# Kernel tuning notes

Measured on AMD Instinct MI355X. Metric: run time of the kernel, lower is better.

## Reference

```python
import jax, jax.numpy as jnp
import numpy as np

N_NODES = 20000   # len(set(idx_i)); edge targets cover all nodes
N_EDGES = 320000
F = 128           # feature dim f
N_RBF = 20        # n radial basis functions
R_CUT = 5.0


def setup_inputs() -> dict:
    key = jax.random.key(0)
    ks = jax.random.split(key, 8)
    s = jax.random.normal(ks[0], (N_EDGES, 1, F), dtype=jnp.float32)
    r = jax.random.normal(ks[1], (N_EDGES, 3), dtype=jnp.float32)
    v = jax.random.normal(ks[2], (N_EDGES, 3, F), dtype=jnp.float32)
    idx_i = jax.random.randint(ks[3], (N_EDGES,), 0, N_NODES, dtype=jnp.int32)
    W_phi = jax.random.normal(ks[4], (F, 3 * F), dtype=jnp.float32) * 0.05
    b_phi = jnp.zeros((3 * F,), dtype=jnp.float32)
    W_w = jax.random.normal(ks[5], (N_RBF, 3 * F), dtype=jnp.float32) * 0.05
    b_w = jnp.zeros((3 * F,), dtype=jnp.float32)
    return {"s": s, "r": r, "v": v, "idx_i": idx_i,
            "W_phi": W_phi, "b_phi": b_phi, "W_w": W_w, "b_w": b_w}


def reference(s, r, v, idx_i, W_phi, b_phi, W_w, b_w):
    # phi network: [E,1,F] -> [E,1,3F]
    phi_out = jnp.einsum('eif,fg->eig', s, W_phi) + b_phi

    # RBF on edge vector norms: [E,1,1] -> [E,1,n]
    r_norm = jnp.linalg.norm(r, axis=1, keepdims=True)[:, :, None]  # [E,1,1]
    n_vals = jnp.arange(1, N_RBF + 1, dtype=jnp.float32)            # [n]
    rbf = jnp.sin(n_vals * (jnp.pi / R_CUT) * r_norm) / r_norm      # [E,1,n]
    # cosine cutoff applied to rbf values (faithful to source)
    rbf = jnp.where(rbf <= R_CUT,
                    0.5 * (jnp.cos(jnp.pi * rbf / R_CUT) + 1.0),
                    jnp.zeros_like(rbf))

    # w network: [E,1,n] -> [E,1,3F]
    w = jnp.einsum('ein,ng->eig', rbf, W_w) + b_w

    split = w * phi_out                    # [E,1,3F]
    sp0 = split[..., :F]                   # gates v
    sp1 = split[..., F:2 * F]              # scalar message
    sp2 = split[..., 2 * F:]               # gates direction

    # scatter-add scalar messages -> [N,1,F]
    out_s = jax.ops.segment_sum(sp1, idx_i, num_segments=N_NODES)

    # direction term: detached r, normalized by GLOBAL Frobenius norm (faithful)
    org_r = jax.lax.stop_gradient(r)
    org_r = org_r / jnp.linalg.norm(org_r)         # [E,3]
    dir_msg = sp2 * org_r[:, :, None]              # [E,3,F]
    v_msg = dir_msg + sp0 * v                      # [E,3,F]

    # scatter-add vector messages -> [N,3,F]
    out_v = jax.ops.segment_sum(v_msg, idx_i, num_segments=N_NODES)
    return out_v, out_s
```

## Files before the change

### kernel.cpp

```cpp
#include <hip/hip_runtime.h>
#include <hip/hip_bf16.h>
#include <math.h>

#define E_TOT   320000
#define NNODE   20000
#define FDIM    128
#define N3F     384
#define NRBF    20
#define OV_SIZE (NNODE * 3 * FDIM)

typedef __attribute__((ext_vector_type(8))) short short8;
typedef __attribute__((ext_vector_type(4))) short short4v;
typedef __attribute__((ext_vector_type(4))) float f32x4;

__device__ __forceinline__ short f2bf(float x) {
  union { float f; unsigned u; } v; v.f = x;
  unsigned r = (v.u + 0x7fffu + ((v.u >> 16) & 1u)) >> 16;
  return (short)r;
}

__global__ void sumsq_kernel(const float* __restrict__ r, float* __restrict__ ws, int n) {
  int tid = blockIdx.x * blockDim.x + threadIdx.x;
  float acc = 0.f;
  for (int i = tid; i < n; i += gridDim.x * blockDim.x) {
    float x = r[i];
    acc += x * x;
  }
  for (int off = 32; off > 0; off >>= 1) acc += __shfl_down(acc, off);
  __shared__ float s[4];
  int lane = threadIdx.x & 63, w = threadIdx.x >> 6;
  if (lane == 0) s[w] = acc;
  __syncthreads();
  if (threadIdx.x == 0) {
    float t = s[0] + s[1] + s[2] + s[3];
    unsafeAtomicAdd(ws, t);
  }
}

__global__ void prep_kernel(const float* __restrict__ Wphi, const float* __restrict__ Ww,
                            short* __restrict__ frag) {
  int g = blockIdx.x * 256 + threadIdx.x;
  int lane = g & 63;
  int fid  = g >> 6;
  short* out = frag + (size_t)g * 8;
  if (fid < 96) {
    int ntile = fid >> 2, ks = fid & 3;
    int n  = ntile * 16 + (lane & 15);
    int kb = ks * 32 + (lane >> 4) * 8;
#pragma unroll
    for (int j = 0; j < 8; ++j) out[j] = f2bf(Wphi[(kb + j) * N3F + n]);
  } else if (fid < 120) {
    int ntile = fid - 96;
    int n  = ntile * 16 + (lane & 15);
    int kb = (lane >> 4) * 8;
#pragma unroll
    for (int j = 0; j < 8; ++j) {
      int k = kb + j;
      out[j] = (k < NRBF) ? f2bf(Ww[k * N3F + n]) : (short)0;
    }
  }
}

__launch_bounds__(256, 2)
__global__ void main_kernel(const float* __restrict__ s_in, const float* __restrict__ r_in,
                            const float* __restrict__ v_in, const int* __restrict__ idx_in,
                            const float* __restrict__ bphi_in, const float* __restrict__ bw_in,
                            const short* __restrict__ frag, const float* __restrict__ ws_sumsq,
                            float* __restrict__ out) {
  __shared__ __align__(16) short sh_s[64 * 136];
  __shared__ __align__(16) short sh_rbf[64 * 40];
  __shared__ float sh_bphi[N3F];
  __shared__ float sh_bw[N3F];
  __shared__ float sh_orgr[64][4];
  __shared__ int   sh_idx[64];

  const int tid = threadIdx.x;
  const int e0  = blockIdx.x * 64;
  const float inv_gnorm = 1.0f / sqrtf(ws_sumsq[0]);

  const float4* s4 = (const float4*)(s_in + (size_t)e0 * FDIM);
#pragma unroll
  for (int it = 0; it < 8; ++it) {
    int idx4 = tid + it * 256;
    float4 val = s4[idx4];
    int e = idx4 >> 5, kq = idx4 & 31;
    short4v p = { f2bf(val.x), f2bf(val.y), f2bf(val.z), f2bf(val.w) };
    *(short4v*)&sh_s[e * 136 + kq * 4] = p;
  }
  for (int j = tid; j < N3F; j += 256) {
    sh_bphi[j] = bphi_in[j];
    sh_bw[j]   = bw_in[j];
  }
  if (tid < 64) {
    int e = e0 + tid;
    sh_idx[tid] = idx_in[e];
    float rx = r_in[e * 3 + 0], ry = r_in[e * 3 + 1], rz = r_in[e * 3 + 2];
    float rn = sqrtf(rx * rx + ry * ry + rz * rz);
    float irn = 1.0f / rn;
    sh_orgr[tid][0] = rx * inv_gnorm;
    sh_orgr[tid][1] = ry * inv_gnorm;
    sh_orgr[tid][2] = rz * inv_gnorm;
    const float c0 = 0.62831853071795864769f;
#pragma unroll
    for (int n = 1; n <= NRBF; ++n) {
      float t = sinf(((float)n * c0) * rn) * irn;
      float val = (t <= 5.0f) ? 0.5f * (cosf(c0 * t) + 1.0f) : 0.0f;
      sh_rbf[tid * 40 + (n - 1)] = f2bf(val);
    }
#pragma unroll
    for (int k = NRBF; k < 32; ++k) sh_rbf[tid * 40 + k] = 0;
  }
  __syncthreads();

  const int wave = tid >> 6, lane = tid & 63;
  const int col  = lane & 15;
  const int q    = lane >> 4;

  const int arow = wave * 16 + col;
  short8 a_phi[4];
#pragma unroll
  for (int ks = 0; ks < 4; ++ks)
    a_phi[ks] = *(const short8*)&sh_s[arow * 136 + ks * 32 + q * 8];
  short8 a_w = *(const short8*)&sh_rbf[arow * 40 + q * 8];

  int   nidx[4]; int erow[4];
  float orx[4], ory[4], orz[4];
#pragma unroll
  for (int i = 0; i < 4; ++i) {
    int el = wave * 16 + q * 4 + i;
    erow[i] = el;
    nidx[i] = sh_idx[el];
    orx[i] = sh_orgr[el][0];
    ory[i] = sh_orgr[el][1];
    orz[i] = sh_orgr[el][2];
  }

  float* out_v = out;
  float* out_s = out + OV_SIZE;
  const short8* fp = (const short8*)frag;
  const short8* fw = fp + 96 * 64;

  for (int f = 0; f < 8; ++f) {
    const int nt0 = f, nt1 = f + 8, nt2 = f + 16;
    f32x4 accP0 = {0.f, 0.f, 0.f, 0.f}, accP1 = accP0, accP2 = accP0;
    f32x4 accW0 = accP0, accW1 = accP0, accW2 = accP0;
#pragma unroll
    for (int ks = 0; ks < 4; ++ks) {
      short8 b0 = fp[(nt0 * 4 + ks) * 64 + lane];
      short8 b1 = fp[(nt1 * 4 + ks) * 64 + lane];
      short8 b2 = fp[(nt2 * 4 + ks) * 64 + lane];
      accP0 = __builtin_amdgcn_mfma_f32_16x16x32_bf16(a_phi[ks], b0, accP0, 0, 0, 0);
      accP1 = __builtin_amdgcn_mfma_f32_16x16x32_bf16(a_phi[ks], b1, accP1, 0, 0, 0);
      accP2 = __builtin_amdgcn_mfma_f32_16x16x32_bf16(a_phi[ks], b2, accP2, 0, 0, 0);
    }
    accW0 = __builtin_amdgcn_mfma_f32_16x16x32_bf16(a_w, fw[nt0 * 64 + lane], accW0, 0, 0, 0);
    accW1 = __builtin_amdgcn_mfma_f32_16x16x32_bf16(a_w, fw[nt1 * 64 + lane], accW1, 0, 0, 0);
    accW2 = __builtin_amdgcn_mfma_f32_16x16x32_bf16(a_w, fw[nt2 * 64 + lane], accW2, 0, 0, 0);

    const int feat = f * 16 + col;
    const float bp0 = sh_bphi[feat], bp1 = sh_bphi[feat + 128], bp2 = sh_bphi[feat + 256];
    const float bw0 = sh_bw[feat],   bw1 = sh_bw[feat + 128],   bw2 = sh_bw[feat + 256];
#pragma unroll
    for (int i = 0; i < 4; ++i) {
      float sp0 = (accW0[i] + bw0) * (accP0[i] + bp0);
      float sp1 = (accW1[i] + bw1) * (accP1[i] + bp1);
      float sp2 = (accW2[i] + bw2) * (accP2[i] + bp2);
      int node = nidx[i];
      unsafeAtomicAdd(&out_s[node * FDIM + feat], sp1);
      const float* vp = v_in + (size_t)(e0 + erow[i]) * (3 * FDIM) + feat;
      unsafeAtomicAdd(&out_v[(node * 3 + 0) * FDIM + feat], sp2 * orx[i] + sp0 * vp[0]);
      unsafeAtomicAdd(&out_v[(node * 3 + 1) * FDIM + feat], sp2 * ory[i] + sp0 * vp[FDIM]);
      unsafeAtomicAdd(&out_v[(node * 3 + 2) * FDIM + feat], sp2 * orz[i] + sp0 * vp[2 * FDIM]);
    }
  }
}

extern "C" void kernel_launch(void* const* d_in, const int* in_sizes, int n_in,
                              void* d_out, int out_size, void* d_ws, size_t ws_size,
                              hipStream_t stream) {
  const float* s_in  = (const float*)d_in[0];
  const float* r_in  = (const float*)d_in[1];
  const float* v_in  = (const float*)d_in[2];
  const int*   idx_i = (const int*)d_in[3];
  const float* Wphi  = (const float*)d_in[4];
  const float* bphi  = (const float*)d_in[5];
  const float* Ww    = (const float*)d_in[6];
  const float* bw    = (const float*)d_in[7];
  float* out = (float*)d_out;

  float* ws_sumsq = (float*)d_ws;
  short* frag     = (short*)((char*)d_ws + 16);

  hipMemsetAsync(d_out, 0, (size_t)out_size * sizeof(float), stream);
  hipMemsetAsync(d_ws, 0, 16, stream);
  sumsq_kernel<<<480, 256, 0, stream>>>(r_in, ws_sumsq, in_sizes[1]);
  prep_kernel<<<30, 256, 0, stream>>>(Wphi, Ww, frag);
  main_kernel<<<E_TOT / 64, 256, 0, stream>>>(s_in, r_in, v_in, idx_i, bphi, bw,
                                              frag, ws_sumsq, out);
}
```

Baseline: 1.158 ms.

## Sort edges by target node and accumulate segments in LDS before global atomics

Adds a counting sort of edges by target node (histogram, scan, scatter), then has the main kernel process edges in sorted order through a permutation. Inside each 64-edge block, runs of the same node are reduced in registers and then in shared memory. Interior nodes get plain stores and only the boundary nodes use global atomics. This is meant to cut global atomic traffic and contention, at the cost of three extra kernels, gathered reads of s, r and v through the permutation, and a fallback path when workspace is too small. Occupancy is also raised to 4 blocks per SM.

```diff
diff --git a/kernel.cpp b/kernel.cpp
--- a/kernel.cpp
+++ b/kernel.cpp
@@ -8,6 +8,7 @@
 #define N3F     384
 #define NRBF    20
 #define OV_SIZE (NNODE * 3 * FDIM)
+#define DMAX    16
 
 typedef __attribute__((ext_vector_type(8))) short short8;
 typedef __attribute__((ext_vector_type(4))) short short4v;
@@ -61,40 +62,67 @@
   }
 }
 
-__launch_bounds__(256, 2)
+__global__ void hist_kernel(const int* __restrict__ idx, int* __restrict__ cnt) {
+  int e = blockIdx.x * 256 + threadIdx.x;
+  if (e < E_TOT) atomicAdd(&cnt[idx[e]], 1);
+}
+
+__global__ void scan_kernel(const int* __restrict__ cnt, int* __restrict__ cursor) {
+  __shared__ int part[256];
+  __shared__ int base_sh[256];
+  const int t = threadIdx.x;
+  int lo = t * 79; if (lo > NNODE) lo = NNODE;
+  int hi = t * 79 + 79; if (hi > NNODE) hi = NNODE;
+  int s = 0;
+  for (int i = lo; i < hi; ++i) s += cnt[i];
+  part[t] = s;
+  __syncthreads();
+  if (t == 0) {
+    int run = 0;
+    for (int i = 0; i < 256; ++i) { base_sh[i] = run; run += part[i]; }
+  }
+  __syncthreads();
+  int run = base_sh[t];
+  for (int i = lo; i < hi; ++i) { cursor[i] = run; run += cnt[i]; }
+}
+
+__global__ void scatter_kernel(const int* __restrict__ idx, int* __restrict__ cursor,
+                               int* __restrict__ perm) {
+  int e = blockIdx.x * 256 + threadIdx.x;
+  if (e < E_TOT) {
+    int p = atomicAdd(&cursor[idx[e]], 1);
+    perm[p] = e;
+  }
+}
+
+template <bool USE_PERM>
+__launch_bounds__(256, 4)
 __global__ void main_kernel(const float* __restrict__ s_in, const float* __restrict__ r_in,
                             const float* __restrict__ v_in, const int* __restrict__ idx_in,
                             const float* __restrict__ bphi_in, const float* __restrict__ bw_in,
                             const short* __restrict__ frag, const float* __restrict__ ws_sumsq,
-                            float* __restrict__ out) {
-  __shared__ __align__(16) short sh_s[64 * 136];
-  __shared__ __align__(16) short sh_rbf[64 * 40];
+                            const int* __restrict__ perm, float* __restrict__ out) {
+  __shared__ __align__(16) char pool[DMAX * 512 * 4];
+  short* sh_s   = (short*)pool;
+  short* sh_rbf = (short*)(pool + 64 * 136 * 2);
+  float* acc    = (float*)pool;
   __shared__ float sh_bphi[N3F];
   __shared__ float sh_bw[N3F];
   __shared__ float sh_orgr[64][4];
-  __shared__ int   sh_idx[64];
+  __shared__ int   sh_perm[64];
+  __shared__ int   sh_lid[64];
+  __shared__ int   sh_nodes[64];
+  __shared__ int   sh_d;
 
   const int tid = threadIdx.x;
   const int e0  = blockIdx.x * 64;
   const float inv_gnorm = 1.0f / sqrtf(ws_sumsq[0]);
 
-  const float4* s4 = (const float4*)(s_in + (size_t)e0 * FDIM);
-#pragma unroll
-  for (int it = 0; it < 8; ++it) {
-    int idx4 = tid + it * 256;
-    float4 val = s4[idx4];
-    int e = idx4 >> 5, kq = idx4 & 31;
-    short4v p = { f2bf(val.x), f2bf(val.y), f2bf(val.z), f2bf(val.w) };
-    *(short4v*)&sh_s[e * 136 + kq * 4] = p;
-  }
-  for (int j = tid; j < N3F; j += 256) {
-    sh_bphi[j] = bphi_in[j];
-    sh_bw[j]   = bw_in[j];
-  }
   if (tid < 64) {
-    int e = e0 + tid;
-    sh_idx[tid] = idx_in[e];
-    float rx = r_in[e * 3 + 0], ry = r_in[e * 3 + 1], rz = r_in[e * 3 + 2];
+    int pe = USE_PERM ? perm[e0 + tid] : (e0 + tid);
+    sh_perm[tid] = pe;
+    int node = idx_in[pe];
+    float rx = r_in[pe * 3 + 0], ry = r_in[pe * 3 + 1], rz = r_in[pe * 3 + 2];
     float rn = sqrtf(rx * rx + ry * ry + rz * rz);
     float irn = 1.0f / rn;
     sh_orgr[tid][0] = rx * inv_gnorm;
@@ -109,6 +137,28 @@
     }
 #pragma unroll
     for (int k = NRBF; k < 32; ++k) sh_rbf[tid * 40 + k] = 0;
+    int prev = __shfl_up(node, 1);
+    int flag = (tid == 0) || (node != prev);
+    unsigned long long m = __ballot(flag);
+    int lid = (int)__popcll(m & ((2ull << tid) - 1ull)) - 1;
+    sh_lid[tid] = lid;
+    if (flag) sh_nodes[lid] = node;
+    if (tid == 0) sh_d = (int)__popcll(m);
+  }
+  for (int j = tid; j < N3F; j += 256) {
+    sh_bphi[j] = bphi_in[j];
+    sh_bw[j]   = bw_in[j];
+  }
+  __syncthreads();
+
+#pragma unroll
+  for (int it = 0; it < 8; ++it) {
+    int idx4 = tid + it * 256;
+    int row = idx4 >> 5, kq = idx4 & 31;
+    const float4* srow = (const float4*)(s_in + (size_t)sh_perm[row] * FDIM);
+    float4 val = srow[kq];
+    short4v p = { f2bf(val.x), f2bf(val.y), f2bf(val.z), f2bf(val.w) };
+    *(short4v*)&sh_s[row * 136 + kq * 4] = p;
   }
   __syncthreads();
 
@@ -123,17 +173,25 @@
     a_phi[ks] = *(const short8*)&sh_s[arow * 136 + ks * 32 + q * 8];
   short8 a_w = *(const short8*)&sh_rbf[arow * 40 + q * 8];
 
-  int   nidx[4]; int erow[4];
+  int   lid4[4]; int vbase[4];
   float orx[4], ory[4], orz[4];
 #pragma unroll
   for (int i = 0; i < 4; ++i) {
     int el = wave * 16 + q * 4 + i;
-    erow[i] = el;
-    nidx[i] = sh_idx[el];
+    lid4[i]  = sh_lid[el];
+    vbase[i] = sh_perm[el] * (3 * FDIM);
     orx[i] = sh_orgr[el][0];
     ory[i] = sh_orgr[el][1];
     orz[i] = sh_orgr[el][2];
   }
+  const int d = sh_d;
+  const bool use_lds = USE_PERM && (d <= DMAX);
+
+  __syncthreads();
+  if (use_lds) {
+    for (int j = tid; j < (d << 9); j += 256) acc[j] = 0.f;
+  }
+  __syncthreads();
 
   float* out_v = out;
   float* out_s = out + OV_SIZE;
@@ -160,17 +218,53 @@
     const int feat = f * 16 + col;
     const float bp0 = sh_bphi[feat], bp1 = sh_bphi[feat + 128], bp2 = sh_bphi[feat + 256];
     const float bw0 = sh_bw[feat],   bw1 = sh_bw[feat + 128],   bw2 = sh_bw[feat + 256];
+
+    auto flush = [&](int l, float as, float avx, float avy, float avz) {
+      if (use_lds) {
+        atomicAdd(&acc[(l << 9) + feat], as);
+        atomicAdd(&acc[(l << 9) + 128 + feat], avx);
+        atomicAdd(&acc[(l << 9) + 256 + feat], avy);
+        atomicAdd(&acc[(l << 9) + 384 + feat], avz);
+      } else {
+        int node = sh_nodes[l];
+        unsafeAtomicAdd(&out_s[node * FDIM + feat], as);
+        unsafeAtomicAdd(&out_v[(node * 3 + 0) * FDIM + feat], avx);
+        unsafeAtomicAdd(&out_v[(node * 3 + 1) * FDIM + feat], avy);
+        unsafeAtomicAdd(&out_v[(node * 3 + 2) * FDIM + feat], avz);
+      }
+    };
+
+    float as = 0.f, avx = 0.f, avy = 0.f, avz = 0.f;
+    int cur = lid4[0];
 #pragma unroll
     for (int i = 0; i < 4; ++i) {
       float sp0 = (accW0[i] + bw0) * (accP0[i] + bp0);
       float sp1 = (accW1[i] + bw1) * (accP1[i] + bp1);
       float sp2 = (accW2[i] + bw2) * (accP2[i] + bp2);
-      int node = nidx[i];
-      unsafeAtomicAdd(&out_s[node * FDIM + feat], sp1);
-      const float* vp = v_in + (size_t)(e0 + erow[i]) * (3 * FDIM) + feat;
-      unsafeAtomicAdd(&out_v[(node * 3 + 0) * FDIM + feat], sp2 * orx[i] + sp0 * vp[0]);
-      unsafeAtomicAdd(&out_v[(node * 3 + 1) * FDIM + feat], sp2 * ory[i] + sp0 * vp[FDIM]);
-      unsafeAtomicAdd(&out_v[(node * 3 + 2) * FDIM + feat], sp2 * orz[i] + sp0 * vp[2 * FDIM]);
+      const float* vp = v_in + (size_t)vbase[i] + feat;
+      float mx = sp2 * orx[i] + sp0 * vp[0];
+      float my = sp2 * ory[i] + sp0 * vp[FDIM];
+      float mz = sp2 * orz[i] + sp0 * vp[2 * FDIM];
+      if (lid4[i] != cur) {
+        flush(cur, as, avx, avy, avz);
+        as = avx = avy = avz = 0.f;
+        cur = lid4[i];
+      }
+      as += sp1; avx += mx; avy += my; avz += mz;
+    }
+    flush(cur, as, avx, avy, avz);
+  }
+
+  if (use_lds) {
+    __syncthreads();
+    for (int j = tid; j < (d << 9); j += 256) {
+      int l = j >> 9, rem = j & 511, comp = rem >> 7, ft = rem & 127;
+      int node = sh_nodes[l];
+      float val = acc[j];
+      float* dst = (comp == 0) ? &out_s[node * FDIM + ft]
+                               : &out_v[(node * 3 + (comp - 1)) * FDIM + ft];
+      if (l > 0 && l < d - 1) *dst = val;
+      else unsafeAtomicAdd(dst, val);
     }
   }
 }
@@ -188,13 +282,29 @@
   const float* bw    = (const float*)d_in[7];
   float* out = (float*)d_out;
 
+  const size_t WS_NEED_SORTED = 1562896;
+  const bool use_sorted = (ws_size >= WS_NEED_SORTED);
+
   float* ws_sumsq = (float*)d_ws;
-  short* frag     = (short*)((char*)d_ws + 16);
+  int*   cnt      = (int*)((char*)d_ws + 16);
+  short* frag_s   = (short*)((char*)d_ws + 80016);
+  int*   cursor   = (int*)((char*)d_ws + 202896);
+  int*   permv    = (int*)((char*)d_ws + 282896);
+  short* frag_f   = (short*)((char*)d_ws + 16);
+  short* frag     = use_sorted ? frag_s : frag_f;
 
   hipMemsetAsync(d_out, 0, (size_t)out_size * sizeof(float), stream);
-  hipMemsetAsync(d_ws, 0, 16, stream);
+  hipMemsetAsync(d_ws, 0, use_sorted ? 80016 : 16, stream);
   sumsq_kernel<<<480, 256, 0, stream>>>(r_in, ws_sumsq, in_sizes[1]);
   prep_kernel<<<30, 256, 0, stream>>>(Wphi, Ww, frag);
-  main_kernel<<<E_TOT / 64, 256, 0, stream>>>(s_in, r_in, v_in, idx_i, bphi, bw,
-                                              frag, ws_sumsq, out);
-}
+  if (use_sorted) {
+    hist_kernel<<<1250, 256, 0, stream>>>(idx_i, cnt);
+    scan_kernel<<<1, 256, 0, stream>>>(cnt, cursor);
+    scatter_kernel<<<1250, 256, 0, stream>>>(idx_i, cursor, permv);
+    main_kernel<true><<<E_TOT / 64, 256, 0, stream>>>(s_in, r_in, v_in, idx_i, bphi, bw,
+                                                      frag, ws_sumsq, permv, out);
+  } else {
+    main_kernel<false><<<E_TOT / 64, 256, 0, stream>>>(s_in, r_in, v_in, idx_i, bphi, bw,
+                                                       frag, ws_sumsq, nullptr, out);
+  }
+}
```

After: 989.8 us. 1.17x faster.
